# Optimization experiments

Measured on AMD Instinct MI355X. Metric: run time of the kernel, lower is better.

Reference implementation:

```python
import jax, jax.numpy as jnp
import numpy as np

N_TOKENS = 32768
EMBED_DIM = 1024
NUM_EXPERTS = 64
TOP_K = 2


def setup_inputs() -> dict:
    key = jax.random.key(0)
    kx, kw = jax.random.split(key)
    x = jax.random.normal(kx, (N_TOKENS, EMBED_DIM), dtype=jnp.float32)
    # nn.Linear(embed_dim, num_experts).weight has shape (num_experts, embed_dim)
    W_gate = jax.random.normal(kw, (NUM_EXPERTS, EMBED_DIM), dtype=jnp.float32) * 0.02
    return {"x": x, "W_gate": W_gate}


def reference(x, W_gate):
    # (N, E) router logits: x @ W.T
    logits = jnp.einsum("nd,ed->ne", x, W_gate)
    probs = jax.nn.softmax(logits, axis=-1)
    top_k_probs, top_k_indices = jax.lax.top_k(probs, TOP_K)
    top_k_probs = top_k_probs / jnp.sum(top_k_probs, axis=-1, keepdims=True)
    # load-balancing aux loss
    expert_mask = jnp.sum(jax.nn.one_hot(top_k_indices, NUM_EXPERTS, dtype=jnp.float32), axis=1)  # (N, E)
    f = jnp.mean(expert_mask, axis=0)  # fraction of tokens routed to each expert (sums to top_k)
    p = jnp.mean(probs, axis=0)        # mean gate prob per expert
    aux_loss = NUM_EXPERTS * jnp.sum(f * p)
    return (top_k_probs, top_k_indices, aux_loss)
```

## Files before the change

### kernel.cpp

```cpp
#include <hip/hip_runtime.h>
#include <cstdint>

#define N_TOK   32768
#define DIM     1024
#define NEXP    64
#define TM      128
#define BK      32
#define KITERS  (DIM / BK)
#define NTHR    256

typedef uint32_t __attribute__((address_space(3))) lds_u32_t;
typedef const uint32_t __attribute__((address_space(1))) glb_u32_t;

__device__ __forceinline__ void gload16(const float* g, float4* l) {
  __builtin_amdgcn_global_load_lds((glb_u32_t*)g, (lds_u32_t*)l, 16, 0, 0);
}

__device__ __forceinline__ int swz(int r, int s) { return (r << 3) + (s ^ ((r >> 2) & 7)); }

__launch_bounds__(NTHR, 1)
__global__ void router_kernel(const float* __restrict__ x,
                              const float* __restrict__ Wg,
                              float* __restrict__ out,
                              unsigned int* __restrict__ cnt_g,
                              float* __restrict__ sp_g) {
  __shared__ float4 Xs4[2][TM * BK / 4];
  __shared__ float4 Ws4[2][NEXP * BK / 4];
  __shared__ float  L[TM * 65];
  __shared__ float  Linv[TM];
  __shared__ float  colpart[4 * NEXP];
  __shared__ unsigned int cnt_s[NEXP];

  const int tid  = threadIdx.x;
  const int tx   = tid & 15;
  const int ty   = tid >> 4;
  const int tok0 = blockIdx.x * TM;

  if (tid < NEXP) cnt_s[tid] = 0;

  int pA[4], pB[2];
  const float* srcA[4];
  const float* srcB[2];
#pragma unroll
  for (int q = 0; q < 4; ++q) {
    int p = q * 256 + tid;
    pA[q] = p;
    int r = p >> 3, sc = p & 7;
    int s = sc ^ ((r >> 2) & 7);
    srcA[q] = x + (size_t)(tok0 + r) * DIM + s * 4;
  }
#pragma unroll
  for (int q = 0; q < 2; ++q) {
    int p = q * 256 + tid;
    pB[q] = p;
    int r = p >> 3, sc = p & 7;
    int s = sc ^ ((r >> 2) & 7);
    srcB[q] = Wg + (size_t)r * DIM + s * 4;
  }

  float acc[8][4];
#pragma unroll
  for (int i = 0; i < 8; ++i)
#pragma unroll
    for (int j = 0; j < 4; ++j) acc[i][j] = 0.f;

#pragma unroll
  for (int q = 0; q < 4; ++q) { gload16(srcA[q], &Xs4[0][pA[q]]); srcA[q] += BK; }
#pragma unroll
  for (int q = 0; q < 2; ++q) { gload16(srcB[q], &Ws4[0][pB[q]]); srcB[q] += BK; }

  for (int it = 0; it < KITERS; ++it) {
    const int b = it & 1;
    if (it < KITERS - 1) {
#pragma unroll
      for (int q = 0; q < 4; ++q) { gload16(srcA[q], &Xs4[b ^ 1][pA[q]]); srcA[q] += BK; }
#pragma unroll
      for (int q = 0; q < 2; ++q) { gload16(srcB[q], &Ws4[b ^ 1][pB[q]]); srcB[q] += BK; }
      asm volatile("s_waitcnt vmcnt(6)" ::: "memory");
    } else {
      asm volatile("s_waitcnt vmcnt(0)" ::: "memory");
    }
    __builtin_amdgcn_s_barrier();
    asm volatile("" ::: "memory");

#pragma unroll
    for (int dd = 0; dd < BK; dd += 4) {
      const int sidx = dd >> 2;
      float4 wv[4];
#pragma unroll
      for (int j = 0; j < 4; ++j) wv[j] = Ws4[b][swz(tx * 4 + j, sidx)];
#pragma unroll
      for (int i = 0; i < 8; ++i) {
        float4 xv = Xs4[b][swz(ty * 8 + i, sidx)];
#pragma unroll
        for (int j = 0; j < 4; ++j) {
          acc[i][j] = fmaf(xv.x, wv[j].x, acc[i][j]);
          acc[i][j] = fmaf(xv.y, wv[j].y, acc[i][j]);
          acc[i][j] = fmaf(xv.z, wv[j].z, acc[i][j]);
          acc[i][j] = fmaf(xv.w, wv[j].w, acc[i][j]);
        }
      }
    }
    asm volatile("" ::: "memory");
    __builtin_amdgcn_s_barrier();
    asm volatile("" ::: "memory");
  }

#pragma unroll
  for (int i = 0; i < 8; ++i)
#pragma unroll
    for (int j = 0; j < 4; ++j)
      L[(ty * 8 + i) * 65 + tx * 4 + j] = acc[i][j];
  __syncthreads();

  if (tid < TM) {
    const int base = tid * 65;
    float v1 = -1e30f, v2 = -1e30f;
    int i1 = 0, i2 = 0;
    for (int e = 0; e < NEXP; ++e) {
      float v = L[base + e];
      if (v > v1)      { v2 = v1; i2 = i1; v1 = v; i1 = e; }
      else if (v > v2) { v2 = v;  i2 = e; }
    }
    float ssum = 0.f;
    for (int e = 0; e < NEXP; ++e) {
      float p = __expf(L[base + e] - v1);
      ssum += p;
      L[base + e] = p;
    }
    Linv[tid] = 1.f / ssum;

    float e2   = __expf(v2 - v1);
    float invn = 1.f / (1.f + e2);
    const int g = tok0 + tid;
    out[2 * g]     = invn;
    out[2 * g + 1] = e2 * invn;
    out[2 * N_TOK + 2 * g]     = (float)i1;
    out[2 * N_TOK + 2 * g + 1] = (float)i2;
    atomicAdd(&cnt_s[i1], 1u);
    atomicAdd(&cnt_s[i2], 1u);
  }
  __syncthreads();

  {
    const int e = tid & 63;
    const int q = tid >> 6;
    float s = 0.f;
#pragma unroll 4
    for (int t = 0; t < 32; ++t) {
      int row = q * 32 + t;
      s += L[row * 65 + e] * Linv[row];
    }
    colpart[q * 64 + e] = s;
  }
  __syncthreads();
  if (tid < NEXP) {
    float tot = colpart[tid] + colpart[64 + tid] + colpart[128 + tid] + colpart[192 + tid];
    atomicAdd(&sp_g[tid], tot);
    atomicAdd(&cnt_g[tid], cnt_s[tid]);
  }
}

__global__ void aux_kernel(const unsigned int* __restrict__ cnt,
                           const float* __restrict__ sp,
                           float* __restrict__ out) {
  const int l = threadIdx.x;
  float v = (float)cnt[l] * sp[l];
#pragma unroll
  for (int off = 32; off > 0; off >>= 1) v += __shfl_down(v, off);
  if (l == 0)
    out[4 * N_TOK] = (float)NEXP * v * (1.f / (float)N_TOK) * (1.f / (float)N_TOK);
}

extern "C" void kernel_launch(void* const* d_in, const int* in_sizes, int n_in,
                              void* d_out, int out_size, void* d_ws, size_t ws_size,
                              hipStream_t stream) {
  const float* x  = (const float*)d_in[0];
  const float* Wg = (const float*)d_in[1];
  float* out = (float*)d_out;
  unsigned int* cnt = (unsigned int*)d_ws;
  float* sp = (float*)((char*)d_ws + 256);

  hipMemsetAsync(d_ws, 0, 512, stream);
  router_kernel<<<dim3(N_TOK / TM), dim3(NTHR), 0, stream>>>(x, Wg, out, cnt, sp);
  aux_kernel<<<dim3(1), dim3(64), 0, stream>>>(cnt, sp, out);
}
```

Baseline: 255.3 us.

## Halve token tile, do softmax/top-k in registers via shuffles, drop global atomics

Shrinks the token tile from 128 to 64 rows, which doubles the block count and allows up to four blocks per CU. The LDS logits buffer and the serial per-token epilogue are replaced by in-register top-2 and softmax, using cross-lane xor shuffles over the 16 threads that share a row. Per-block partial sums are written to workspace and reduced by a 256-thread aux kernel, which removes the memset and the global atomics when the workspace is large enough. In exchange, the smaller tile gives less reuse of W per loaded x, and the aux kernel now has more partials to reduce.

```diff
diff --git a/kernel.cpp b/kernel.cpp
--- a/kernel.cpp
+++ b/kernel.cpp
@@ -4,10 +4,11 @@
 #define N_TOK   32768
 #define DIM     1024
 #define NEXP    64
-#define TM      128
+#define TM      64
 #define BK      32
 #define KITERS  (DIM / BK)
 #define NTHR    256
+#define NBLK    (N_TOK / TM)
 
 typedef uint32_t __attribute__((address_space(3))) lds_u32_t;
 typedef const uint32_t __attribute__((address_space(1))) glb_u32_t;
@@ -18,16 +19,15 @@
 
 __device__ __forceinline__ int swz(int r, int s) { return (r << 3) + (s ^ ((r >> 2) & 7)); }
 
-__launch_bounds__(NTHR, 1)
+template<bool PART>
+__launch_bounds__(NTHR, 4)
 __global__ void router_kernel(const float* __restrict__ x,
                               const float* __restrict__ Wg,
                               float* __restrict__ out,
-                              unsigned int* __restrict__ cnt_g,
+                              float* __restrict__ cnt_g,
                               float* __restrict__ sp_g) {
   __shared__ float4 Xs4[2][TM * BK / 4];
   __shared__ float4 Ws4[2][NEXP * BK / 4];
-  __shared__ float  L[TM * 65];
-  __shared__ float  Linv[TM];
   __shared__ float  colpart[4 * NEXP];
   __shared__ unsigned int cnt_s[NEXP];
 
@@ -38,11 +38,11 @@
 
   if (tid < NEXP) cnt_s[tid] = 0;
 
-  int pA[4], pB[2];
-  const float* srcA[4];
+  int pA[2], pB[2];
+  const float* srcA[2];
   const float* srcB[2];
 #pragma unroll
-  for (int q = 0; q < 4; ++q) {
+  for (int q = 0; q < 2; ++q) {
     int p = q * 256 + tid;
     pA[q] = p;
     int r = p >> 3, sc = p & 7;
@@ -58,14 +58,14 @@
     srcB[q] = Wg + (size_t)r * DIM + s * 4;
   }
 
-  float acc[8][4];
-#pragma unroll
-  for (int i = 0; i < 8; ++i)
+  float acc[4][4];
+#pragma unroll
+  for (int i = 0; i < 4; ++i)
 #pragma unroll
     for (int j = 0; j < 4; ++j) acc[i][j] = 0.f;
 
 #pragma unroll
-  for (int q = 0; q < 4; ++q) { gload16(srcA[q], &Xs4[0][pA[q]]); srcA[q] += BK; }
+  for (int q = 0; q < 2; ++q) { gload16(srcA[q], &Xs4[0][pA[q]]); srcA[q] += BK; }
 #pragma unroll
   for (int q = 0; q < 2; ++q) { gload16(srcB[q], &Ws4[0][pB[q]]); srcB[q] += BK; }
 
@@ -73,10 +73,10 @@
     const int b = it & 1;
     if (it < KITERS - 1) {
 #pragma unroll
-      for (int q = 0; q < 4; ++q) { gload16(srcA[q], &Xs4[b ^ 1][pA[q]]); srcA[q] += BK; }
+      for (int q = 0; q < 2; ++q) { gload16(srcA[q], &Xs4[b ^ 1][pA[q]]); srcA[q] += BK; }
 #pragma unroll
       for (int q = 0; q < 2; ++q) { gload16(srcB[q], &Ws4[b ^ 1][pB[q]]); srcB[q] += BK; }
-      asm volatile("s_waitcnt vmcnt(6)" ::: "memory");
+      asm volatile("s_waitcnt vmcnt(4)" ::: "memory");
     } else {
       asm volatile("s_waitcnt vmcnt(0)" ::: "memory");
     }
@@ -90,8 +90,8 @@
 #pragma unroll
       for (int j = 0; j < 4; ++j) wv[j] = Ws4[b][swz(tx * 4 + j, sidx)];
 #pragma unroll
-      for (int i = 0; i < 8; ++i) {
-        float4 xv = Xs4[b][swz(ty * 8 + i, sidx)];
+      for (int i = 0; i < 4; ++i) {
+        float4 xv = Xs4[b][swz(ty * 4 + i, sidx)];
 #pragma unroll
         for (int j = 0; j < 4; ++j) {
           acc[i][j] = fmaf(xv.x, wv[j].x, acc[i][j]);
@@ -106,70 +106,100 @@
     asm volatile("" ::: "memory");
   }
 
-#pragma unroll
-  for (int i = 0; i < 8; ++i)
-#pragma unroll
-    for (int j = 0; j < 4; ++j)
-      L[(ty * 8 + i) * 65 + tx * 4 + j] = acc[i][j];
+  float sp_loc[4] = {0.f, 0.f, 0.f, 0.f};
+
+#pragma unroll
+  for (int i = 0; i < 4; ++i) {
+    float v1 = acc[i][0]; int e1 = tx * 4;
+    float v2 = -3.4e38f;  int e2 = 0;
+#pragma unroll
+    for (int j = 1; j < 4; ++j) {
+      float v = acc[i][j]; int e = tx * 4 + j;
+      if (v > v1)      { v2 = v1; e2 = e1; v1 = v; e1 = e; }
+      else if (v > v2) { v2 = v;  e2 = e; }
+    }
+#pragma unroll
+    for (int m = 1; m <= 8; m <<= 1) {
+      float b1 = __shfl_xor(v1, m), b2 = __shfl_xor(v2, m);
+      int   f1 = __shfl_xor(e1, m), f2 = __shfl_xor(e2, m);
+      bool bwin = (b1 > v1) || (b1 == v1 && f1 < e1);
+      if (bwin) {
+        bool keep = (v1 > b2) || (v1 == b2 && e1 < f2);
+        v2 = keep ? v1 : b2; e2 = keep ? e1 : f2;
+        v1 = b1; e1 = f1;
+      } else {
+        bool rep = (b1 > v2) || (b1 == v2 && f1 < e2);
+        v2 = rep ? b1 : v2; e2 = rep ? f1 : e2;
+      }
+    }
+    float s = 0.f;
+#pragma unroll
+    for (int j = 0; j < 4; ++j) { float e = __expf(acc[i][j] - v1); acc[i][j] = e; s += e; }
+#pragma unroll
+    for (int m = 1; m <= 8; m <<= 1) s += __shfl_xor(s, m);
+    float inv = 1.f / s;
+#pragma unroll
+    for (int j = 0; j < 4; ++j) sp_loc[j] += acc[i][j] * inv;
+
+    if (tx == 0) {
+      int g = tok0 + ty * 4 + i;
+      float e2v = __expf(v2 - v1);
+      float r = 1.f / (1.f + e2v);
+      out[2 * g]     = r;
+      out[2 * g + 1] = e2v * r;
+      out[2 * N_TOK + 2 * g]     = (float)e1;
+      out[2 * N_TOK + 2 * g + 1] = (float)e2;
+      atomicAdd(&cnt_s[e1], 1u);
+      atomicAdd(&cnt_s[e2], 1u);
+    }
+  }
+
+#pragma unroll
+  for (int j = 0; j < 4; ++j) {
+    sp_loc[j] += __shfl_down(sp_loc[j], 32);
+    sp_loc[j] += __shfl_down(sp_loc[j], 16);
+  }
+  const int lane = tid & 63;
+  const int wv_i = tid >> 6;
+  if (lane < 16) {
+#pragma unroll
+    for (int j = 0; j < 4; ++j) colpart[wv_i * 64 + tx * 4 + j] = sp_loc[j];
+  }
   __syncthreads();
 
-  if (tid < TM) {
-    const int base = tid * 65;
-    float v1 = -1e30f, v2 = -1e30f;
-    int i1 = 0, i2 = 0;
-    for (int e = 0; e < NEXP; ++e) {
-      float v = L[base + e];
-      if (v > v1)      { v2 = v1; i2 = i1; v1 = v; i1 = e; }
-      else if (v > v2) { v2 = v;  i2 = e; }
-    }
-    float ssum = 0.f;
-    for (int e = 0; e < NEXP; ++e) {
-      float p = __expf(L[base + e] - v1);
-      ssum += p;
-      L[base + e] = p;
-    }
-    Linv[tid] = 1.f / ssum;
-
-    float e2   = __expf(v2 - v1);
-    float invn = 1.f / (1.f + e2);
-    const int g = tok0 + tid;
-    out[2 * g]     = invn;
-    out[2 * g + 1] = e2 * invn;
-    out[2 * N_TOK + 2 * g]     = (float)i1;
-    out[2 * N_TOK + 2 * g + 1] = (float)i2;
-    atomicAdd(&cnt_s[i1], 1u);
-    atomicAdd(&cnt_s[i2], 1u);
-  }
+  if (tid < NEXP) {
+    float t = colpart[tid] + colpart[64 + tid] + colpart[128 + tid] + colpart[192 + tid];
+    if (PART) {
+      sp_g[(size_t)blockIdx.x * NEXP + tid]  = t;
+      cnt_g[(size_t)blockIdx.x * NEXP + tid] = (float)cnt_s[tid];
+    } else {
+      atomicAdd(&sp_g[tid], t);
+      atomicAdd(&cnt_g[tid], (float)cnt_s[tid]);
+    }
+  }
+}
+
+__global__ void aux_kernel(const float* __restrict__ cnt_p,
+                           const float* __restrict__ sp_p,
+                           float* __restrict__ out, int nb) {
+  __shared__ float redc[256], reds[256];
+  const int t = threadIdx.x, e = t & 63, q = t >> 6;
+  float sc = 0.f, ss = 0.f;
+  for (int b = q; b < nb; b += 4) {
+    sc += cnt_p[b * NEXP + e];
+    ss += sp_p[b * NEXP + e];
+  }
+  redc[t] = sc; reds[t] = ss;
   __syncthreads();
-
-  {
-    const int e = tid & 63;
-    const int q = tid >> 6;
-    float s = 0.f;
-#pragma unroll 4
-    for (int t = 0; t < 32; ++t) {
-      int row = q * 32 + t;
-      s += L[row * 65 + e] * Linv[row];
-    }
-    colpart[q * 64 + e] = s;
-  }
-  __syncthreads();
-  if (tid < NEXP) {
-    float tot = colpart[tid] + colpart[64 + tid] + colpart[128 + tid] + colpart[192 + tid];
-    atomicAdd(&sp_g[tid], tot);
-    atomicAdd(&cnt_g[tid], cnt_s[tid]);
-  }
-}
-
-__global__ void aux_kernel(const unsigned int* __restrict__ cnt,
-                           const float* __restrict__ sp,
-                           float* __restrict__ out) {
-  const int l = threadIdx.x;
-  float v = (float)cnt[l] * sp[l];
-#pragma unroll
-  for (int off = 32; off > 0; off >>= 1) v += __shfl_down(v, off);
-  if (l == 0)
-    out[4 * N_TOK] = (float)NEXP * v * (1.f / (float)N_TOK) * (1.f / (float)N_TOK);
+  if (t < NEXP) {
+    float C = redc[t] + redc[64 + t] + redc[128 + t] + redc[192 + t];
+    float S = reds[t] + reds[64 + t] + reds[128 + t] + reds[192 + t];
+    float v = C * S;
+#pragma unroll
+    for (int off = 32; off; off >>= 1) v += __shfl_down(v, off);
+    if (t == 0)
+      out[4 * N_TOK] = (float)NEXP * v * (1.f / (float)N_TOK) * (1.f / (float)N_TOK);
+  }
 }
 
 extern "C" void kernel_launch(void* const* d_in, const int* in_sizes, int n_in,
@@ -178,10 +208,18 @@
   const float* x  = (const float*)d_in[0];
   const float* Wg = (const float*)d_in[1];
   float* out = (float*)d_out;
-  unsigned int* cnt = (unsigned int*)d_ws;
-  float* sp = (float*)((char*)d_ws + 256);
-
-  hipMemsetAsync(d_ws, 0, 512, stream);
-  router_kernel<<<dim3(N_TOK / TM), dim3(NTHR), 0, stream>>>(x, Wg, out, cnt, sp);
-  aux_kernel<<<dim3(1), dim3(64), 0, stream>>>(cnt, sp, out);
-}
+
+  const size_t need = (size_t)NBLK * NEXP * 2 * sizeof(float);
+  if (ws_size >= need) {
+    float* cnt_p = (float*)d_ws;
+    float* sp_p  = cnt_p + (size_t)NBLK * NEXP;
+    router_kernel<true><<<dim3(NBLK), dim3(NTHR), 0, stream>>>(x, Wg, out, cnt_p, sp_p);
+    aux_kernel<<<dim3(1), dim3(256), 0, stream>>>(cnt_p, sp_p, out, NBLK);
+  } else {
+    float* cnt_p = (float*)d_ws;
+    float* sp_p  = cnt_p + NEXP;
+    hipMemsetAsync(d_ws, 0, 2 * NEXP * sizeof(float), stream);
+    router_kernel<false><<<dim3(NBLK), dim3(NTHR), 0, stream>>>(x, Wg, out, cnt_p, sp_p);
+    aux_kernel<<<dim3(1), dim3(256), 0, stream>>>(cnt_p, sp_p, out, 1);
+  }
+}
```

Measured after the change: 283.7 us. +11.1%, slower.
